# Kernel tuning notes

Hardware: AMD Instinct MI355X
Metric: run time of the kernel (lower is better)

Reference implementation:

```python
import math
import jax, jax.numpy as jnp
import numpy as np

# ---- config (from ModelConfig) ----
HIDDEN = 2880
HEAD_DIM = 64
N_HEADS = 64
N_KV = 8
Q_MULT = N_HEADS // N_KV  # 8
SLIDING_WINDOW = 128      # left context; causal windowed attention
ROPE_BASE = 150000.0
ROPE_SCALE = 32.0
NTK_ALPHA = 1.0
NTK_BETA = 32.0
INIT_CTX = 4096
RMS_EPS = 1e-5
SM_SCALE = 1.0 / math.sqrt(HEAD_DIM)
Q_DIM = N_HEADS * HEAD_DIM   # 4096
KV_DIM = N_KV * HEAD_DIM     # 512
QKV_DIM = Q_DIM + 2 * KV_DIM # 5120
B, T = 1, 2048


def _rope_cos_sin(n_tokens):
    """YaRN-scaled rotary cache, per RotaryEmbedding._compute_concentration_and_inv_freq."""
    d_half = HEAD_DIM // 2
    freq = ROPE_BASE ** (jnp.arange(0, HEAD_DIM, 2, dtype=jnp.float32) / HEAD_DIM)
    concentration = 0.1 * math.log(ROPE_SCALE) + 1.0
    low = d_half * math.log(INIT_CTX / (NTK_BETA * 2 * math.pi)) / math.log(ROPE_BASE)
    high = d_half * math.log(INIT_CTX / (NTK_ALPHA * 2 * math.pi)) / math.log(ROPE_BASE)
    interpolation = 1.0 / (ROPE_SCALE * freq)
    extrapolation = 1.0 / freq
    ramp = (jnp.arange(d_half, dtype=jnp.float32) - low) / (high - low)
    mask = 1.0 - jnp.clip(ramp, 0.0, 1.0)
    inv_freq = interpolation * (1.0 - mask) + extrapolation * mask
    pos = jnp.arange(n_tokens, dtype=jnp.float32)
    angles = pos[:, None] * inv_freq[None, :]  # [t, d/2]
    return jnp.cos(angles) * concentration, jnp.sin(angles) * concentration


def _apply_rope(x, cos, sin):
    """Interleaved RoPE (matches _apply_rotary_emb). x: [b, t, ..., d]."""
    shape = x.shape
    n_mid = x.ndim - 3  # dims between token axis and feature axis
    c = cos.reshape((1, shape[1]) + (1,) * n_mid + (shape[-1] // 2,))
    s = sin.reshape((1, shape[1]) + (1,) * n_mid + (shape[-1] // 2,))
    x1 = x[..., ::2]
    x2 = x[..., 1::2]
    o1 = x1 * c - x2 * s
    o2 = x2 * c + x1 * s
    return jnp.stack((o1, o2), axis=-1).reshape(shape)


def _rmsnorm(x, scale):
    t = x.astype(jnp.float32)
    t = t * jax.lax.rsqrt(jnp.mean(t * t, axis=-1, keepdims=True) + RMS_EPS)
    return (t * scale).astype(x.dtype)


def setup_inputs() -> dict:
    key = jax.random.key(0)
    ks = jax.random.split(key, 7)
    x = jax.random.normal(ks[0], (B, T, HIDDEN), dtype=jnp.float32)
    norm_scale = jnp.ones((HIDDEN,), dtype=jnp.float32)
    w_qkv = jax.random.normal(ks[1], (QKV_DIM, HIDDEN), dtype=jnp.float32) * (HIDDEN ** -0.5)
    b_qkv = jax.random.normal(ks[2], (QKV_DIM,), dtype=jnp.float32) * 0.02
    sinks = jax.random.normal(ks[3], (N_HEADS,), dtype=jnp.float32)
    w_out = jax.random.normal(ks[4], (HIDDEN, Q_DIM), dtype=jnp.float32) * (Q_DIM ** -0.5)
    b_out = jax.random.normal(ks[5], (HIDDEN,), dtype=jnp.float32) * 0.02
    return {"x": x, "norm_scale": norm_scale, "w_qkv": w_qkv, "b_qkv": b_qkv,
            "sinks": sinks, "w_out": w_out, "b_out": b_out}


def reference(x, norm_scale, w_qkv, b_qkv, sinks, w_out, b_out):
    b, t, _ = x.shape
    h = _rmsnorm(x, norm_scale)
    qkv = h @ w_qkv.T + b_qkv  # [b, t, 5120]
    q = qkv[..., :Q_DIM].reshape(b, t, N_KV, Q_MULT, HEAD_DIM)
    k = qkv[..., Q_DIM:Q_DIM + KV_DIM].reshape(b, t, N_KV, HEAD_DIM)
    v = qkv[..., Q_DIM + KV_DIM:].reshape(b, t, N_KV, HEAD_DIM)

    cos, sin = _rope_cos_sin(t)
    q = _apply_rope(q, cos, sin)
    k = _apply_rope(k, cos, sin)

    # sliding-window causal attention with sink logits (sdpa windowed path)
    left_ctx = SLIDING_WINDOW
    window = left_ctx + 1
    kp = jnp.pad(k, ((0, 0), (left_ctx, 0), (0, 0), (0, 0)))
    vp = jnp.pad(v, ((0, 0), (left_ctx, 0), (0, 0), (0, 0)))
    gather_idx = jnp.arange(t)[:, None] + jnp.arange(window)[None, :]  # into padded axis
    kwin = kp[:, gather_idx]  # [b, t, w, n_kv, d]
    vwin = vp[:, gather_idx]

    pos = jnp.arange(t)[:, None] + (jnp.arange(window) - left_ctx)[None, :]
    valid = (pos >= 0) & (pos < t)  # [t, w]

    scores = jnp.einsum('bthqd,btwhd->bthqw', q, kwin).astype(jnp.float32) * SM_SCALE
    scores = jnp.where(valid[None, :, None, None, :], scores, -jnp.inf)

    sink = (sinks * math.log(2.0)).reshape(N_KV, Q_MULT)
    sink = jnp.broadcast_to(sink[None, None, :, :, None], (b, t, N_KV, Q_MULT, 1))
    scores = jnp.concatenate([scores, sink], axis=-1)  # [b, t, h, q, w+1]

    w_attn = jax.nn.softmax(scores, axis=-1)[..., :-1].astype(v.dtype)
    attn = jnp.einsum('bthqw,btwhd->bthqd', w_attn, vwin).reshape(b, t, -1)

    out = attn @ w_out.T + b_out
    return x + out
```

## Files before the change

kernel.cpp:

```cpp
#include <hip/hip_runtime.h>
#include <math.h>

typedef unsigned short u16;
typedef unsigned int   u32;
using f32x4  = __attribute__((ext_vector_type(4))) float;
using bf16x8 = __attribute__((ext_vector_type(8))) __bf16;

#define HIDDEN   2880
#define QKVD     5120
#define QD       4096
#define TTOK     2048
#define NKV      8
#define QMULT    8
#define HD       64
#define NPAD     2944

#define PREP_QKV_BLOCKS  14400
#define PREP_WOUT_BLOCKS 11776
#define PREP_RMS_BLOCKS  2048

static __device__ __forceinline__ float bflo(u32 u){ return __uint_as_float(u << 16); }
static __device__ __forceinline__ float bfhi(u32 u){ return __uint_as_float(u & 0xffff0000u); }
static __device__ __forceinline__ u16 f2bf(float f){
    u32 u = __float_as_uint(f);
    u32 r = (u + 0x7fffu + ((u >> 16) & 1u)) >> 16;
    return (u16)r;
}

static __device__ __forceinline__ void glds16(const void* g, void* l) {
    __builtin_amdgcn_global_load_lds(
        (__attribute__((address_space(1))) void*)g,
        (__attribute__((address_space(3))) void*)l,
        16, 0, 0);
}

#define BAR() asm volatile("s_barrier" ::: "memory")

__global__ __launch_bounds__(256) void prep_kernel(const float* __restrict__ w_qkv,
                                                   u16* __restrict__ wqkv_bf,
                                                   const float* __restrict__ w_out,
                                                   u16* __restrict__ wout_bf,
                                                   const float* __restrict__ x,
                                                   const float* __restrict__ scale,
                                                   u16* __restrict__ h) {
    const int b = blockIdx.x;
    const int tid = threadIdx.x;
    if (b < PREP_QKV_BLOCKS) {
        int i = b * 256 + tid;
        float4 f = ((const float4*)w_qkv)[i];
        ushort4 o;
        o.x = f2bf(f.x); o.y = f2bf(f.y); o.z = f2bf(f.z); o.w = f2bf(f.w);
        ((ushort4*)wqkv_bf)[i] = o;
    } else if (b < PREP_QKV_BLOCKS + PREP_WOUT_BLOCKS) {
        int i = (b - PREP_QKV_BLOCKS) * 256 + tid;
        int idx = i * 4;
        int row = idx >> 12;
        int col = idx & 4095;
        ushort4 o;
        if (row < HIDDEN) {
            float4 f = *(const float4*)(w_out + (long)row * QD + col);
            o.x = f2bf(f.x); o.y = f2bf(f.y); o.z = f2bf(f.z); o.w = f2bf(f.w);
        } else {
            o.x = 0; o.y = 0; o.z = 0; o.w = 0;
        }
        ((ushort4*)wout_bf)[i] = o;
    } else {
        const int t = b - (PREP_QKV_BLOCKS + PREP_WOUT_BLOCKS);
        const float4* xr = (const float4*)(x + (long)t * HIDDEN);
        float4 v[3];
        float ss = 0.f;
        #pragma unroll
        for (int it = 0; it < 3; ++it) {
            int i4 = tid + it * 256;
            if (i4 < 720) {
                v[it] = xr[i4];
                ss += v[it].x*v[it].x + v[it].y*v[it].y + v[it].z*v[it].z + v[it].w*v[it].w;
            }
        }
        #pragma unroll
        for (int off = 32; off > 0; off >>= 1) ss += __shfl_down(ss, off);
        __shared__ float red[4];
        if ((tid & 63) == 0) red[tid >> 6] = ss;
        __syncthreads();
        float tot = red[0] + red[1] + red[2] + red[3];
        float rr = rsqrtf(tot * (1.0f / HIDDEN) + 1e-5f);
        ushort4* hr = (ushort4*)(h + (long)t * HIDDEN);
        #pragma unroll
        for (int it = 0; it < 3; ++it) {
            int i4 = tid + it * 256;
            if (i4 < 720) {
                float4 s4 = ((const float4*)scale)[i4];
                ushort4 o;
                o.x = f2bf(v[it].x * rr * s4.x);
                o.y = f2bf(v[it].y * rr * s4.y);
                o.z = f2bf(v[it].z * rr * s4.z);
                o.w = f2bf(v[it].w * rr * s4.w);
                hr[i4] = o;
            }
        }
    }
}


#define LOAD_AQ(MH) do { \
    aq[0][0] = *(const bf16x8*)(aS + (2*(MH)+0)*2048 + off0); \
    aq[0][1] = *(const bf16x8*)(aS + (2*(MH)+0)*2048 + off1); \
    aq[1][0] = *(const bf16x8*)(aS + (2*(MH)+1)*2048 + off0); \
    aq[1][1] = *(const bf16x8*)(aS + (2*(MH)+1)*2048 + off1); \
} while (0)

#define MFMA_Q(MH) do { \
    __builtin_amdgcn_s_setprio(1); \
    _Pragma("unroll") \
    for (int i2_ = 0; i2_ < 2; ++i2_) { \
        _Pragma("unroll") \
        for (int ni_ = 0; ni_ < 4; ++ni_) { \
            acc[2*(MH)+i2_][ni_] = __builtin_amdgcn_mfma_f32_16x16x32_bf16(aq[i2_][0], bq[ni_][0], acc[2*(MH)+i2_][ni_], 0, 0, 0); \
            acc[2*(MH)+i2_][ni_] = __builtin_amdgcn_mfma_f32_16x16x32_bf16(aq[i2_][1], bq[ni_][1], acc[2*(MH)+i2_][ni_], 0, 0, 0); \
        } \
    } \
    __builtin_amdgcn_s_setprio(0); \
} while (0)

__global__ __launch_bounds__(512, 2) void gemm_bt_8ph(const u16* __restrict__ A,
                                                      const u16* __restrict__ B,
                                                      u16* __restrict__ C0,
                                                      int N, int K, int ksplit,
                                                      int blimit, int colmax) {
    extern __shared__ u16 smem[];
    u16* const smA = smem;
    u16* const smB = smem + 2 * 256 * 64;
    const int tid  = threadIdx.x;
    const int lane = tid & 63;
    const int wv   = tid >> 6;
    const int wm   = wv >> 2;
    const int wn   = wv & 3;
    const long m0  = (long)blockIdx.y * 256;
    const long n0  = (long)blockIdx.x * 256;
    const int kbase = blockIdx.z * ksplit;
    const int NT   = ksplit >> 6;
    u16* C = C0 + (size_t)blockIdx.z * ((size_t)TTOK * N);

    const int srow = tid >> 3;
    const int sg8  = ((tid & 7) ^ (srow & 7)) << 3;
    const int fr   = lane & 15;
    const int off0 = ((lane >> 4) << 4) ^ ((lane & 7) << 4);
    const int off1 = off0 ^ 64;
    const char* aR = (const char*)smA + (wm * 128 + fr) * 128;
    const char* bR = (const char*)smB + (wn * 64  + fr) * 128;

    f32x4 acc[8][4];
    #pragma unroll
    for (int i = 0; i < 8; ++i)
        #pragma unroll
        for (int j = 0; j < 4; ++j) acc[i][j] = f32x4{0.f, 0.f, 0.f, 0.f};

    const u16* Asrc = A + (m0 + srow) * (long)K + kbase + sg8;
    auto stageA = [&](int t) {
        char* dst = (char*)smA + (t & 1) * 32768 + (wv * 8) * 128;
        const u16* src = Asrc + t * 64;
        #pragma unroll
        for (int hj = 0; hj < 4; ++hj)
            glds16(src + (size_t)(hj * 64) * K, dst + hj * 64 * 128);
    };
    auto stageB = [&](int t, int h) {
        char* dst = (char*)smB + (t & 1) * 32768 + (h * 128 + wv * 8) * 128;
        #pragma unroll
        for (int j = 0; j < 2; ++j) {
            long r = n0 + h * 128 + j * 64 + srow;
            if (r > blimit) r = blimit;
            glds16(B + (size_t)r * K + kbase + t * 64 + sg8, dst + j * 64 * 128);
        }
    };

    stageA(0);
    stageB(0, 0); stageB(0, 1);
    if (NT > 1) { stageB(1, 0); stageB(1, 1); }
    if (NT < 3) asm volatile("s_waitcnt vmcnt(0)" ::: "memory");
    else        asm volatile("s_waitcnt vmcnt(4)" ::: "memory");
    BAR();

    for (int t = 0; t < NT; ++t) {
        const int sof = (t & 1) * 32768;
        const char* aS = aR + sof;
        const char* bS = bR + sof;
        bf16x8 bq[4][2], aq[2][2];
        #pragma unroll
        for (int ni = 0; ni < 4; ++ni) {
            bq[ni][0] = *(const bf16x8*)(bS + ni * 2048 + off0);
            bq[ni][1] = *(const bf16x8*)(bS + ni * 2048 + off1);
        }
        LOAD_AQ(0);
        if (t + 1 < NT) stageA(t + 1);
        BAR();
        MFMA_Q(0);
        BAR();
        LOAD_AQ(1);
        if (t + 2 < NT) stageB(t + 2, 0);
        BAR();
        MFMA_Q(1);
        BAR();
        LOAD_AQ(2);
        if (t + 2 < NT) stageB(t + 2, 1);
        BAR();
        MFMA_Q(2);
        BAR();
        LOAD_AQ(3);
        BAR();
        MFMA_Q(3);
        if (t >= NT - 2) asm volatile("s_waitcnt vmcnt(0)" ::: "memory");
        else             asm volatile("s_waitcnt vmcnt(4)" ::: "memory");
        BAR();
    }

    const int cr = (lane >> 4) * 4;
    const int cc = lane & 15;
    #pragma unroll
    for (int ni = 0; ni < 4; ++ni) {
        long col = n0 + wn * 64 + ni * 16 + cc;
        if (col < colmax) {
            #pragma unroll
            for (int mi = 0; mi < 8; ++mi) {
                long row = m0 + wm * 128 + mi * 16 + cr;
                #pragma unroll
                for (int r2 = 0; r2 < 4; ++r2)
                    C[(row + r2) * (long)N + col] = f2bf(acc[mi][ni][r2]);
            }
        }
    }
}

__global__ __launch_bounds__(256) void rope_kernel(const u16* __restrict__ p1,
                                                   const float* __restrict__ b_qkv,
                                                   u16* __restrict__ qr,
                                                   u16* __restrict__ kr,
                                                   u16* __restrict__ vr) {
    const int t = blockIdx.x;
    const int tid = threadIdx.x;
    __shared__ float cs[32], sn[32];
    if (tid < 32) {
        float fi = (float)tid;
        float freq   = exp2f(17.1946032f * (fi * (1.0f / 32.0f)));
        float interp = 1.0f / (32.0f * freq);
        float extra  = 1.0f / freq;
        float ramp   = (fi - 8.0927802f) * (1.0f / (17.3980220f - 8.0927802f));
        float rc     = fminf(fmaxf(ramp, 0.0f), 1.0f);
        float invf   = interp * rc + extra * (1.0f - rc);
        float ang    = (float)t * invf;
        cs[tid] = cosf(ang) * 1.3465736f;
        sn[tid] = sinf(ang) * 1.3465736f;
    }
    __syncthreads();
    const u16* rowA = p1 + (long)t * QKVD;
    auto pair = [&](int col) -> float2 {
        u32 ua = *(const u32*)(rowA + col);
        float2 bb = *(const float2*)(b_qkv + col);
        return make_float2(bflo(ua) + bb.x, bfhi(ua) + bb.y);
    };
    for (int p = tid; p < 2048; p += 256) {
        int hd2 = p >> 5, i = p & 31;
        float2 ab = pair(hd2 * 64 + 2 * i);
        float o1 = ab.x * cs[i] - ab.y * sn[i];
        float o2 = ab.y * cs[i] + ab.x * sn[i];
        *(u32*)(qr + (long)t * QD + hd2 * 64 + 2 * i) = (u32)f2bf(o1) | ((u32)f2bf(o2) << 16);
    }
    {
        int kv = tid >> 5, i = tid & 31;
        float2 ab = pair(QD + kv * 64 + 2 * i);
        float o1 = ab.x * cs[i] - ab.y * sn[i];
        float o2 = ab.y * cs[i] + ab.x * sn[i];
        *(u32*)(kr + ((long)kv * TTOK + t) * HD + 2 * i) = (u32)f2bf(o1) | ((u32)f2bf(o2) << 16);
    }
    {
        int kv = tid >> 5, d2 = tid & 31;
        float2 ab = pair(QD + 512 + kv * 64 + 2 * d2);
        *(u32*)(vr + ((long)kv * TTOK + t) * HD + 2 * d2) = (u32)f2bf(ab.x) | ((u32)f2bf(ab.y) << 16);
    }
}

__global__ __launch_bounds__(256, 2) void attn_kernel(const u16* __restrict__ qr,
                                                      const u16* __restrict__ kr,
                                                      const u16* __restrict__ vr,
                                                      const float* __restrict__ sinks,
                                                      u16* __restrict__ o) {
    const int t0  = blockIdx.x * 16;
    const int h   = blockIdx.y;
    const int qhg = blockIdx.z;
    const int tid = threadIdx.x;
    const int lane = tid & 63, wv = tid >> 6;
    __shared__ __align__(16) u16 ks[144][72];
    __shared__ __align__(16) u16 Vt[64][168];
    __shared__ __align__(16) u16 P [4][16][168];
    const u16* kb = kr + (long)h * TTOK * HD;
    const u16* vb = vr + (long)h * TTOK * HD;

    #pragma unroll
    for (int i = 0; i < 5; ++i) {
        int idx = i * 256 + tid;
        if (idx < 144 * 8) {
            int rr = idx >> 3, c = idx & 7;
            int tk = t0 - 128 + rr;
            int tks = tk < 0 ? 0 : tk;
            *(uint4*)&ks[rr][c * 8] = *(const uint4*)(kb + (long)tks * HD + c * 8);
        }
    }
    #pragma unroll
    for (int c4 = 0; c4 < 8; ++c4) {
        if (tid < 144) {
            int tk = t0 - 128 + tid;
            int tks = tk < 0 ? 0 : tk;
            uint4 v4 = *(const uint4*)(vb + (long)tks * HD + c4 * 8);
            int d0 = c4 * 8;
            Vt[d0+0][tid] = (u16)(v4.x & 0xffff); Vt[d0+1][tid] = (u16)(v4.x >> 16);
            Vt[d0+2][tid] = (u16)(v4.y & 0xffff); Vt[d0+3][tid] = (u16)(v4.y >> 16);
            Vt[d0+4][tid] = (u16)(v4.z & 0xffff); Vt[d0+5][tid] = (u16)(v4.z >> 16);
            Vt[d0+6][tid] = (u16)(v4.w & 0xffff); Vt[d0+7][tid] = (u16)(v4.w >> 16);
        }
    }
    if (tid < 128) {
        *(uint4*)&Vt[tid >> 1][144 + (tid & 1) * 8] = uint4{0, 0, 0, 0};
    }
    if (lane < 32) {
        *(uint4*)&P[wv][lane >> 1][144 + (lane & 1) * 8] = uint4{0, 0, 0, 0};
    }
    __syncthreads();

    const int qh   = qhg * 4 + wv;
    const int head = h * QMULT + qh;
    const int fr = lane & 15, fk = (lane >> 4) * 8;
    const int cr = (lane >> 4) * 4;

    const u16* qrow = qr + (long)(t0 + fr) * QD + head * HD;
    bf16x8 qf0 = *(const bf16x8*)(qrow + fk);
    bf16x8 qf1 = *(const bf16x8*)(qrow + 32 + fk);

    const int kmin = 128 - t0;
    float lsum[4] = {0.f, 0.f, 0.f, 0.f};

    for (int nt = 0; nt < 9; ++nt) {
        bf16x8 b0 = *(const bf16x8*)&ks[nt * 16 + fr][fk];
        bf16x8 b1 = *(const bf16x8*)&ks[nt * 16 + fr][32 + fk];
        f32x4 s = f32x4{0.f, 0.f, 0.f, 0.f};
        s = __builtin_amdgcn_mfma_f32_16x16x32_bf16(qf0, b0, s, 0, 0, 0);
        s = __builtin_amdgcn_mfma_f32_16x16x32_bf16(qf1, b1, s, 0, 0, 0);
        const int kk = nt * 16 + fr;
        #pragma unroll
        for (int r = 0; r < 4; ++r) {
            int row = cr + r;
            bool valid = (kk >= row) && (kk <= row + 128) && (kk >= kmin);
            float p = valid ? __expf(s[r] * 0.125f) : 0.0f;
            lsum[r] += p;
            P[wv][row][kk] = f2bf(p);
        }
    }

    f32x4 oacc[4];
    #pragma unroll
    for (int dt = 0; dt < 4; ++dt) oacc[dt] = f32x4{0.f, 0.f, 0.f, 0.f};
    #pragma unroll
    for (int k5 = 0; k5 < 5; ++k5) {
        const int k0 = k5 * 32;
        bf16x8 pa = *(const bf16x8*)&P[wv][fr][k0 + fk];
        #pragma unroll
        for (int dt = 0; dt < 4; ++dt) {
            bf16x8 vf = *(const bf16x8*)&Vt[dt * 16 + fr][k0 + fk];
            oacc[dt] = __builtin_amdgcn_mfma_f32_16x16x32_bf16(pa, vf, oacc[dt], 0, 0, 0);
        }
    }

    #pragma unroll
    for (int r = 0; r < 4; ++r) {
        float v = lsum[r];
        v += __shfl_xor(v, 1);
        v += __shfl_xor(v, 2);
        v += __shfl_xor(v, 4);
        v += __shfl_xor(v, 8);
        lsum[r] = v;
    }
    const float sk = exp2f(sinks[head]);
    float inv[4];
    #pragma unroll
    for (int r = 0; r < 4; ++r) inv[r] = 1.0f / (lsum[r] + sk);

    #pragma unroll
    for (int dt = 0; dt < 4; ++dt) {
        #pragma unroll
        for (int r = 0; r < 4; ++r) {
            o[(long)(t0 + cr + r) * QD + head * HD + dt * 16 + fr] = f2bf(oacc[dt][r] * inv[r]);
        }
    }
}

__global__ __launch_bounds__(256) void reduce2_kernel(const u16* __restrict__ p2a,
                                                      const u16* __restrict__ p2b,
                                                      const float* __restrict__ x,
                                                      const float* __restrict__ b_out,
                                                      float* __restrict__ out) {
    const int row = blockIdx.y;
    const int c4 = blockIdx.x * 256 + threadIdx.x;
    if (c4 >= 720) return;
    const int col = c4 * 4;
    ushort4 ua = *(const ushort4*)(p2a + (long)row * NPAD + col);
    ushort4 ub = *(const ushort4*)(p2b + (long)row * NPAD + col);
    float4 xv = *(const float4*)(x + (long)row * HIDDEN + col);
    float4 bv = *(const float4*)(b_out + col);
    float4 o;
    o.x = xv.x + bv.x + __uint_as_float((u32)ua.x << 16) + __uint_as_float((u32)ub.x << 16);
    o.y = xv.y + bv.y + __uint_as_float((u32)ua.y << 16) + __uint_as_float((u32)ub.y << 16);
    o.z = xv.z + bv.z + __uint_as_float((u32)ua.z << 16) + __uint_as_float((u32)ub.z << 16);
    o.w = xv.w + bv.w + __uint_as_float((u32)ua.w << 16) + __uint_as_float((u32)ub.w << 16);
    *(float4*)(out + (long)row * HIDDEN + col) = o;
}

extern "C" void kernel_launch(void* const* d_in, const int* in_sizes, int n_in,
                              void* d_out, int out_size, void* d_ws, size_t ws_size,
                              hipStream_t stream) {
    const float* x      = (const float*)d_in[0];
    const float* nscale = (const float*)d_in[1];
    const float* w_qkv  = (const float*)d_in[2];
    const float* b_qkv  = (const float*)d_in[3];
    const float* sinks  = (const float*)d_in[4];
    const float* w_out  = (const float*)d_in[5];
    const float* b_out  = (const float*)d_in[6];
    float* out = (float*)d_out;

    static int smem_set = 0;
    if (!smem_set) {
        hipFuncSetAttribute((const void*)gemm_bt_8ph,
                            hipFuncAttributeMaxDynamicSharedMemorySize, 131072);
        smem_set = 1;
    }

    char* ws = (char*)d_ws;
    size_t off = 0;
    auto alloc = [&](size_t bytes) { void* p = ws + off; off += (bytes + 255) & ~(size_t)255; return p; };
    u16* wqkv_bf = (u16*)alloc((size_t)QKVD * HIDDEN * 2);
    u16* wout_bf = (u16*)alloc((size_t)NPAD * QD * 2);
    u16* h       = (u16*)alloc((size_t)TTOK * HIDDEN * 2);
    u16* p1      = (u16*)alloc((size_t)2 * TTOK * QKVD * 2);
    u16* qrot    = (u16*)alloc((size_t)TTOK * QD * 2);
    u16* krot    = (u16*)alloc((size_t)NKV * TTOK * HD * 2);
    u16* vrot    = (u16*)alloc((size_t)NKV * TTOK * HD * 2);
    u16* attn = wqkv_bf;
    u16* p2   = p1;

    prep_kernel<<<PREP_QKV_BLOCKS + PREP_WOUT_BLOCKS + PREP_RMS_BLOCKS, 256, 0, stream>>>(
        w_qkv, wqkv_bf, w_out, wout_bf, x, nscale, h);
    gemm_bt_8ph<<<dim3(QKVD / 256, TTOK / 256, 1), 512, 131072, stream>>>(
        h, wqkv_bf, p1, QKVD, HIDDEN, HIDDEN, QKVD - 1, QKVD);
    rope_kernel<<<TTOK, 256, 0, stream>>>(p1, b_qkv, qrot, krot, vrot);
    attn_kernel<<<dim3(TTOK / 16, NKV, 2), 256, 0, stream>>>(qrot, krot, vrot, sinks, attn);
    gemm_bt_8ph<<<dim3((NPAD + 255) / 256, TTOK / 256, 2), 512, 131072, stream>>>(
        attn, wout_bf, p2, NPAD, QD, QD / 2, NPAD - 1, NPAD);
    reduce2_kernel<<<dim3(3, TTOK), 256, 0, stream>>>(
        p2, p2 + (size_t)TTOK * NPAD, x, b_out, out);
}
```

Measured before the change: 345.3 us.

## Overlap w_out conversion with QKV GEMM and triple-buffer A tiles

Moves the fp32-to-bf16 conversion of w_out out of the prep kernel and into extra z-slices of the QKV GEMM launch, so the conversion can run concurrently with GEMM blocks instead of serially before them. The GEMM A operand staging also goes from double to triple buffering, prefetching two k-steps ahead, which raises dynamic LDS per block to 160 KB. The larger LDS footprint may cut resident blocks per CU, and the conversion blocks still compete with the GEMM for bandwidth and CU slots.

```diff
diff --git a/kernel.cpp b/kernel.cpp
--- a/kernel.cpp
+++ b/kernel.cpp
@@ -16,7 +16,6 @@
 #define NPAD     2944
 
 #define PREP_QKV_BLOCKS  14400
-#define PREP_WOUT_BLOCKS 11776
 #define PREP_RMS_BLOCKS  2048
 
 static __device__ __forceinline__ float bflo(u32 u){ return __uint_as_float(u << 16); }
@@ -38,8 +37,6 @@
 
 __global__ __launch_bounds__(256) void prep_kernel(const float* __restrict__ w_qkv,
                                                    u16* __restrict__ wqkv_bf,
-                                                   const float* __restrict__ w_out,
-                                                   u16* __restrict__ wout_bf,
                                                    const float* __restrict__ x,
                                                    const float* __restrict__ scale,
                                                    u16* __restrict__ h) {
@@ -51,21 +48,8 @@
         ushort4 o;
         o.x = f2bf(f.x); o.y = f2bf(f.y); o.z = f2bf(f.z); o.w = f2bf(f.w);
         ((ushort4*)wqkv_bf)[i] = o;
-    } else if (b < PREP_QKV_BLOCKS + PREP_WOUT_BLOCKS) {
-        int i = (b - PREP_QKV_BLOCKS) * 256 + tid;
-        int idx = i * 4;
-        int row = idx >> 12;
-        int col = idx & 4095;
-        ushort4 o;
-        if (row < HIDDEN) {
-            float4 f = *(const float4*)(w_out + (long)row * QD + col);
-            o.x = f2bf(f.x); o.y = f2bf(f.y); o.z = f2bf(f.z); o.w = f2bf(f.w);
-        } else {
-            o.x = 0; o.y = 0; o.z = 0; o.w = 0;
-        }
-        ((ushort4*)wout_bf)[i] = o;
     } else {
-        const int t = b - (PREP_QKV_BLOCKS + PREP_WOUT_BLOCKS);
+        const int t = b - PREP_QKV_BLOCKS;
         const float4* xr = (const float4*)(x + (long)t * HIDDEN);
         float4 v[3];
         float ss = 0.f;
@@ -126,11 +110,37 @@
                                                       const u16* __restrict__ B,
                                                       u16* __restrict__ C0,
                                                       int N, int K, int ksplit,
-                                                      int blimit, int colmax) {
+                                                      int blimit, int colmax,
+                                                      int nz_gemm,
+                                                      const float* __restrict__ wout_src,
+                                                      u16* __restrict__ wout_dst) {
+    const int tid  = threadIdx.x;
+
+    if ((int)blockIdx.z >= nz_gemm) {
+        const long nb = (long)gridDim.x * gridDim.y;
+        long bidx = (long)blockIdx.y * gridDim.x + blockIdx.x;
+        long i = bidx * 512 + tid;
+        const long tot = (long)NPAD * QD / 4;
+        const long stride = nb * 512;
+        for (; i < tot; i += stride) {
+            long idx = i * 4;
+            int row = (int)(idx >> 12);
+            int col = (int)(idx & 4095);
+            ushort4 o;
+            if (row < HIDDEN) {
+                float4 f = *(const float4*)(wout_src + (long)row * QD + col);
+                o.x = f2bf(f.x); o.y = f2bf(f.y); o.z = f2bf(f.z); o.w = f2bf(f.w);
+            } else {
+                o.x = 0; o.y = 0; o.z = 0; o.w = 0;
+            }
+            ((ushort4*)wout_dst)[i] = o;
+        }
+        return;
+    }
+
     extern __shared__ u16 smem[];
     u16* const smA = smem;
-    u16* const smB = smem + 2 * 256 * 64;
-    const int tid  = threadIdx.x;
+    u16* const smB = smem + 3 * 256 * 64;
     const int lane = tid & 63;
     const int wv   = tid >> 6;
     const int wm   = wv >> 2;
@@ -156,8 +166,8 @@
         for (int j = 0; j < 4; ++j) acc[i][j] = f32x4{0.f, 0.f, 0.f, 0.f};
 
     const u16* Asrc = A + (m0 + srow) * (long)K + kbase + sg8;
-    auto stageA = [&](int t) {
-        char* dst = (char*)smA + (t & 1) * 32768 + (wv * 8) * 128;
+    auto stageA = [&](int t, int slot) {
+        char* dst = (char*)smA + slot * 32768 + (wv * 8) * 128;
         const u16* src = Asrc + t * 64;
         #pragma unroll
         for (int hj = 0; hj < 4; ++hj)
@@ -173,17 +183,18 @@
         }
     };
 
-    stageA(0);
+    stageA(0, 0);
     stageB(0, 0); stageB(0, 1);
-    if (NT > 1) { stageB(1, 0); stageB(1, 1); }
-    if (NT < 3) asm volatile("s_waitcnt vmcnt(0)" ::: "memory");
-    else        asm volatile("s_waitcnt vmcnt(4)" ::: "memory");
+    if (NT > 1) { stageA(1, 1); stageB(1, 0); stageB(1, 1); }
+    if (NT > 1) asm volatile("s_waitcnt vmcnt(8)" ::: "memory");
+    else        asm volatile("s_waitcnt vmcnt(0)" ::: "memory");
     BAR();
 
+    int sA = 0;
     for (int t = 0; t < NT; ++t) {
-        const int sof = (t & 1) * 32768;
-        const char* aS = aR + sof;
-        const char* bS = bR + sof;
+        const char* aS = aR + sA * 32768;
+        const char* bS = bR + (t & 1) * 32768;
+        int sA2 = sA + 2; if (sA2 >= 3) sA2 -= 3;
         bf16x8 bq[4][2], aq[2][2];
         #pragma unroll
         for (int ni = 0; ni < 4; ++ni) {
@@ -191,7 +202,7 @@
             bq[ni][1] = *(const bf16x8*)(bS + ni * 2048 + off1);
         }
         LOAD_AQ(0);
-        if (t + 1 < NT) stageA(t + 1);
+        if (t + 2 < NT) stageA(t + 2, sA2);
         BAR();
         MFMA_Q(0);
         BAR();
@@ -208,9 +219,10 @@
         LOAD_AQ(3);
         BAR();
         MFMA_Q(3);
-        if (t >= NT - 2) asm volatile("s_waitcnt vmcnt(0)" ::: "memory");
-        else             asm volatile("s_waitcnt vmcnt(4)" ::: "memory");
-        BAR();
+        if (t + 2 < NT)      asm volatile("s_waitcnt vmcnt(8)" ::: "memory");
+        else if (t + 1 < NT) asm volatile("s_waitcnt vmcnt(0)" ::: "memory");
+        BAR();
+        sA = (sA == 2) ? 0 : sA + 1;
     }
 
     const int cr = (lane >> 4) * 4;
@@ -427,7 +439,7 @@
     static int smem_set = 0;
     if (!smem_set) {
         hipFuncSetAttribute((const void*)gemm_bt_8ph,
-                            hipFuncAttributeMaxDynamicSharedMemorySize, 131072);
+                            hipFuncAttributeMaxDynamicSharedMemorySize, 163840);
         smem_set = 1;
     }
 
@@ -444,14 +456,14 @@
     u16* attn = wqkv_bf;
     u16* p2   = p1;
 
-    prep_kernel<<<PREP_QKV_BLOCKS + PREP_WOUT_BLOCKS + PREP_RMS_BLOCKS, 256, 0, stream>>>(
-        w_qkv, wqkv_bf, w_out, wout_bf, x, nscale, h);
-    gemm_bt_8ph<<<dim3(QKVD / 256, TTOK / 256, 1), 512, 131072, stream>>>(
-        h, wqkv_bf, p1, QKVD, HIDDEN, HIDDEN, QKVD - 1, QKVD);
+    prep_kernel<<<PREP_QKV_BLOCKS + PREP_RMS_BLOCKS, 256, 0, stream>>>(
+        w_qkv, wqkv_bf, x, nscale, h);
+    gemm_bt_8ph<<<dim3(QKVD / 256, TTOK / 256, 2), 512, 163840, stream>>>(
+        h, wqkv_bf, p1, QKVD, HIDDEN, HIDDEN, QKVD - 1, QKVD, 1, w_out, wout_bf);
     rope_kernel<<<TTOK, 256, 0, stream>>>(p1, b_qkv, qrot, krot, vrot);
     attn_kernel<<<dim3(TTOK / 16, NKV, 2), 256, 0, stream>>>(qrot, krot, vrot, sinks, attn);
-    gemm_bt_8ph<<<dim3((NPAD + 255) / 256, TTOK / 256, 2), 512, 131072, stream>>>(
-        attn, wout_bf, p2, NPAD, QD, QD / 2, NPAD - 1, NPAD);
+    gemm_bt_8ph<<<dim3((NPAD + 255) / 256, TTOK / 256, 2), 512, 163840, stream>>>(
+        attn, wout_bf, p2, NPAD, QD, QD / 2, NPAD - 1, NPAD, 2, nullptr, nullptr);
     reduce2_kernel<<<dim3(3, TTOK), 256, 0, stream>>>(
         p2, p2 + (size_t)TTOK * NPAD, x, b_out, out);
 }
```

Result: faster. 334.3 us (-3.2%).
